# Optimization experiments

Hardware: AMD Instinct MI355X
Metric: run time of the kernel (lower is better)

## Reference

```python
import jax, jax.numpy as jnp
import numpy as np

EPS = 1e-5
HEADS = 16
DIM_HEAD = 64
ROPE_THETA = 10000.0


def layer_norm(x, g, b):
    mu = x.mean(-1, keepdims=True)
    var = x.var(-1, keepdims=True)
    return (x - mu) / jnp.sqrt(var + EPS) * g + b


def apply_rope(t):
    # t: [b, h, n, d]; interleaved-pair RoPE (rotary-embedding-torch default)
    n, d = t.shape[-2], t.shape[-1]
    inv_freq = 1.0 / (ROPE_THETA ** (jnp.arange(0, d, 2, dtype=jnp.float32) / d))  # [d/2]
    freqs = jnp.arange(n, dtype=jnp.float32)[:, None] * inv_freq[None, :]          # [n, d/2]
    freqs = jnp.repeat(freqs, 2, axis=-1)                                          # [n, d]
    cos, sin = jnp.cos(freqs).astype(t.dtype), jnp.sin(freqs).astype(t.dtype)
    t2 = t.reshape(*t.shape[:-1], d // 2, 2)
    t_rot = jnp.stack((-t2[..., 1], t2[..., 0]), axis=-1).reshape(t.shape)
    return t * cos + t_rot * sin


def setup_inputs() -> dict:
    key = jax.random.key(0)
    k0, k1, k2 = jax.random.split(key, 3)
    B, N, D = 1, 4096, 1024
    inner = HEADS * DIM_HEAD
    x = jax.random.normal(k0, (B, N, D), jnp.float32)
    w_qkv = jax.random.normal(k1, (D, inner * 3), jnp.float32) * (D ** -0.5)
    w_out = jax.random.normal(k2, (inner, D), jnp.float32) * (inner ** -0.5)
    ln_g = jnp.ones((D,), jnp.float32)
    ln_b = jnp.zeros((D,), jnp.float32)
    return {"x": x, "w_qkv": w_qkv, "w_out": w_out, "ln_g": ln_g, "ln_b": ln_b}


def reference(x, w_qkv, w_out, ln_g, ln_b):
    B, N, D = x.shape
    H, DH = HEADS, DIM_HEAD
    scale = DH ** -0.5

    h = layer_norm(x, ln_g, ln_b)
    qkv = h @ w_qkv                                    # [b, n, 3*inner]
    q, k, v = jnp.split(qkv, 3, axis=-1)
    to_heads = lambda t: t.reshape(B, N, H, DH).transpose(0, 2, 1, 3)  # [b,h,n,d]
    q, k, v = to_heads(q), to_heads(k), to_heads(v)

    new_k, new_v = k, v  # cache holds pre-RoPE k, v (as in original)

    q = apply_rope(q)
    k = apply_rope(k)

    dots = jnp.einsum('bhid,bhjd->bhij', q, k) * scale  # [b,h,n,n]
    causal_mask = jnp.triu(jnp.ones((N, N), dtype=bool), 1)
    dots = jnp.where(causal_mask, -jnp.inf, dots)
    attn = jax.nn.softmax(dots, axis=-1)
    out = jnp.einsum('bhij,bhjd->bhid', attn, v)        # [b,h,n,d]
    out = out.transpose(0, 2, 1, 3).reshape(B, N, H * DH)
    return out @ w_out, new_k, new_v
```

## Files before the change

### kernel.cpp

```cpp
#include <hip/hip_runtime.h>
#include <math.h>

#define D_MODEL 1024
#define N_SEQ   4096
#define N_HEADS 16
#define DHEAD   64
#define QKV_COLS 3072

typedef short bf16x8 __attribute__((ext_vector_type(8)));
typedef short bf16x4 __attribute__((ext_vector_type(4)));
typedef float f32x4  __attribute__((ext_vector_type(4)));

#define MFMA32(a, b, c) __builtin_amdgcn_mfma_f32_16x16x32_bf16(a, b, c, 0, 0, 0)
#define MFMA16(a, b, c) __builtin_amdgcn_mfma_f32_16x16x16bf16_1k(a, b, c, 0, 0, 0)

static __device__ __forceinline__ unsigned short f2bf(float f) {
    union { float f; unsigned u; } v; v.f = f;
    unsigned r = (v.u + 0x7fffu + ((v.u >> 16) & 1u)) >> 16;
    return (unsigned short)r;
}

static __device__ __forceinline__ bf16x4 pack_bf16x4(float a, float b, float c, float d) {
    union { float f; unsigned u; } x0, x1, x2, x3;
    x0.f = a; x1.f = b; x2.f = c; x3.f = d;
    union { unsigned u[2]; bf16x4 v; } r;
    r.u[0] = __builtin_amdgcn_perm(x1.u, x0.u, 0x07060302u);
    r.u[1] = __builtin_amdgcn_perm(x3.u, x2.u, 0x07060302u);
    return r.v;
}

typedef __attribute__((address_space(1))) const void* gas_t;
typedef __attribute__((address_space(3))) void* las_t;
static __device__ __forceinline__ void load_lds16(const unsigned short* g, unsigned short* l) {
    __builtin_amdgcn_global_load_lds((gas_t)g, (las_t)l, 16, 0, 0);
}

static __device__ __forceinline__ void fast_sincos(float theta, float* s, float* c) {
    float rev = theta * 0.15915494309189535f;
    rev = rev - floorf(rev);
    float a = rev * 6.283185307179586f;
    *s = __sinf(a);
    *c = __cosf(a);
}

__constant__ unsigned char U_TAB[80] = {
    71,65,59,54,49,45,40,36,31,27,23,19,15,11,7,3,
    69,63,57,52,48,43,39,34,30,26,22,18,14,10,6,2,
    67,61,55,51,46,42,37,33,29,25,21,17,13,9,5,1,
    70,68,66,64,53,50,47,44,28,24,20,16,79,78,77,76,
    56,58,60,62,32,35,38,41,0,4,8,12,72,73,74,75
};

__global__ __launch_bounds__(256) void ln_kernel(const float* __restrict__ x,
                                                 const float* __restrict__ g,
                                                 const float* __restrict__ b,
                                                 unsigned short* __restrict__ h) {
    int row = blockIdx.x;
    int t = threadIdx.x;
    float4 v = ((const float4*)(x + (size_t)row * D_MODEL))[t];
    float s  = v.x + v.y + v.z + v.w;
    float ss = v.x*v.x + v.y*v.y + v.z*v.z + v.w*v.w;
    for (int off = 32; off; off >>= 1) {
        s  += __shfl_down(s, off);
        ss += __shfl_down(ss, off);
    }
    __shared__ float sm[4], ssm[4];
    __shared__ float mu_s, rs_s;
    int wave = t >> 6, lane = t & 63;
    if (lane == 0) { sm[wave] = s; ssm[wave] = ss; }
    __syncthreads();
    if (t == 0) {
        float S = 0.f, SS = 0.f;
        for (int w = 0; w < 4; w++) { S += sm[w]; SS += ssm[w]; }
        float mu = S / D_MODEL;
        float var = SS / D_MODEL - mu * mu;
        mu_s = mu;
        rs_s = rsqrtf(var + 1e-5f);
    }
    __syncthreads();
    float mu = mu_s, rs = rs_s;
    float4 gv = ((const float4*)g)[t];
    float4 bv = ((const float4*)b)[t];
    ushort4 o;
    o.x = f2bf((v.x - mu) * rs * gv.x + bv.x);
    o.y = f2bf((v.y - mu) * rs * gv.y + bv.y);
    o.z = f2bf((v.z - mu) * rs * gv.z + bv.z);
    o.w = f2bf((v.w - mu) * rs * gv.w + bv.w);
    *(ushort4*)(h + (size_t)row * D_MODEL + t * 4) = o;
}

__global__ __launch_bounds__(256) void transpose_cvt2(const float* __restrict__ Wa,
                                                      unsigned short* __restrict__ Ta,
                                                      const float* __restrict__ Wb,
                                                      unsigned short* __restrict__ Tb) {
    __shared__ float tile[64][65];
    int by = blockIdx.y;
    const float* W; unsigned short* Wt; int N, n0;
    if (by < 48) { W = Wa; Wt = Ta; N = QKV_COLS; n0 = by * 64; }
    else         { W = Wb; Wt = Tb; N = D_MODEL;  n0 = (by - 48) * 64; }
    const int K = D_MODEL;
    int k0 = blockIdx.x * 64;
    int t = threadIdx.x;
#pragma unroll
    for (int p = 0; p < 16; p++) {
        int idx = p * 256 + t;
        int r = idx >> 6, c = idx & 63;
        tile[r][c] = W[(size_t)(k0 + r) * N + n0 + c];
    }
    __syncthreads();
#pragma unroll
    for (int p = 0; p < 16; p++) {
        int idx = p * 256 + t;
        int r2 = idx >> 6, c2 = idx & 63;
        Wt[(size_t)(n0 + r2) * K + k0 + c2] = f2bf(tile[c2][r2]);
    }
}

__global__ __launch_bounds__(256) void gemm_bt128(const unsigned short* __restrict__ A,
                                                  const unsigned short* __restrict__ Bt,
                                                  float* __restrict__ C,
                                                  int M, int N, int K) {
    __shared__ unsigned short As[128 * 32];
    __shared__ unsigned short Bs[128 * 32];
    int t = threadIdx.x;
    int w = t >> 6, lane = t & 63;
    int l16 = lane & 15, quad = lane >> 4;
    int wr = w >> 1, wc = w & 1;
    int m0 = blockIdx.x * 128, n0 = blockIdx.y * 128;
    int srow = lane >> 2, scol = (lane & 3) * 8;
    int c0 = w * 2, c1 = c0 + 1;

    f32x4 acc[4][4] = {};

    for (int k0 = 0; k0 < K; k0 += 32) {
        __syncthreads();
        load_lds16(A  + (size_t)(m0 + c0 * 16 + srow) * K + k0 + scol, &As[c0 * 512 + lane * 8]);
        load_lds16(A  + (size_t)(m0 + c1 * 16 + srow) * K + k0 + scol, &As[c1 * 512 + lane * 8]);
        load_lds16(Bt + (size_t)(n0 + c0 * 16 + srow) * K + k0 + scol, &Bs[c0 * 512 + lane * 8]);
        load_lds16(Bt + (size_t)(n0 + c1 * 16 + srow) * K + k0 + scol, &Bs[c1 * 512 + lane * 8]);
        __syncthreads();
        bf16x8 a[4], b[4];
#pragma unroll
        for (int mt = 0; mt < 4; mt++)
            a[mt] = *(const bf16x8*)&As[(wr * 64 + mt * 16 + l16) * 32 + quad * 8];
#pragma unroll
        for (int nt = 0; nt < 4; nt++)
            b[nt] = *(const bf16x8*)&Bs[(wc * 64 + nt * 16 + l16) * 32 + quad * 8];
#pragma unroll
        for (int mt = 0; mt < 4; mt++)
#pragma unroll
            for (int nt = 0; nt < 4; nt++)
                acc[mt][nt] = MFMA32(a[mt], b[nt], acc[mt][nt]);
    }
#pragma unroll
    for (int mt = 0; mt < 4; mt++)
#pragma unroll
        for (int nt = 0; nt < 4; nt++)
#pragma unroll
            for (int r = 0; r < 4; r++)
                C[(size_t)(m0 + wr * 64 + mt * 16 + quad * 4 + r) * N + n0 + wc * 64 + nt * 16 + l16] =
                    acc[mt][nt][r];
}

__global__ __launch_bounds__(256) void gemm_bt64(const unsigned short* __restrict__ A,
                                                 const unsigned short* __restrict__ Bt,
                                                 float* __restrict__ C,
                                                 int M, int N, int K) {
    __shared__ unsigned short As[64 * 32];
    __shared__ unsigned short Bs[128 * 32];
    int t = threadIdx.x;
    int w = t >> 6, lane = t & 63;
    int l16 = lane & 15, quad = lane >> 4;
    int wr = w >> 1, wc = w & 1;
    int m0 = blockIdx.x * 64, n0 = blockIdx.y * 128;
    int srow = lane >> 2, scol = (lane & 3) * 8;
    int c0 = w * 2, c1 = c0 + 1;
    int srow2 = t >> 2, scol2 = (t & 3) * 8;

    f32x4 acc[2][4] = {};

    for (int k0 = 0; k0 < K; k0 += 32) {
        __syncthreads();
        load_lds16(A  + (size_t)(m0 + srow2) * K + k0 + scol2, &As[t * 8]);
        load_lds16(Bt + (size_t)(n0 + c0 * 16 + srow) * K + k0 + scol, &Bs[c0 * 512 + lane * 8]);
        load_lds16(Bt + (size_t)(n0 + c1 * 16 + srow) * K + k0 + scol, &Bs[c1 * 512 + lane * 8]);
        __syncthreads();
        bf16x8 a[2], b[4];
#pragma unroll
        for (int mt = 0; mt < 2; mt++)
            a[mt] = *(const bf16x8*)&As[(wr * 32 + mt * 16 + l16) * 32 + quad * 8];
#pragma unroll
        for (int nt = 0; nt < 4; nt++)
            b[nt] = *(const bf16x8*)&Bs[(wc * 64 + nt * 16 + l16) * 32 + quad * 8];
#pragma unroll
        for (int mt = 0; mt < 2; mt++)
#pragma unroll
            for (int nt = 0; nt < 4; nt++)
                acc[mt][nt] = MFMA32(a[mt], b[nt], acc[mt][nt]);
    }
#pragma unroll
    for (int mt = 0; mt < 2; mt++)
#pragma unroll
        for (int nt = 0; nt < 4; nt++)
#pragma unroll
            for (int r = 0; r < 4; r++)
                C[(size_t)(m0 + wr * 32 + mt * 16 + quad * 4 + r) * N + n0 + wc * 64 + nt * 16 + l16] =
                    acc[mt][nt][r];
}

__global__ __launch_bounds__(256) void rope_cache_kernel(const float* __restrict__ qkv,
                                                         float* __restrict__ out_k,
                                                         float* __restrict__ out_v,
                                                         unsigned short* __restrict__ q_bf,
                                                         unsigned short* __restrict__ k_bf,
                                                         unsigned short* __restrict__ vt_bf) {
    __shared__ unsigned short Vt[64 * 72];
    int nt = blockIdx.x, h = blockIdx.y;
    int n0 = nt * 64;
    int t = threadIdx.x;
    int row = t >> 2;
    int n = n0 + row;
    const float* src = qkv + (size_t)n * QKV_COLS + h * 64;
    size_t nd_base = ((size_t)h * N_SEQ + n) * 64;
    const float QSCALE = 0.18033688011112042f;
    const float NL2_32 = -0.41524101186092029f;
#pragma unroll
    for (int j = 0; j < 4; j++) {
        int c = (t & 3) * 4 + j * 16;
        float4 q4 = *(const float4*)(src + c);
        float4 k4 = *(const float4*)(src + 1024 + c);
        float4 v4 = *(const float4*)(src + 2048 + c);
        *(float4*)(out_k + nd_base + c) = k4;
        *(float4*)(out_v + nd_base + c) = v4;
        float i0 = (float)(c >> 1), i1 = i0 + 1.f;
        float if0 = exp2f(i0 * NL2_32);
        float if1 = exp2f(i1 * NL2_32);
        float s0, c0s, s1, c1s;
        fast_sincos((float)n * if0, &s0, &c0s);
        fast_sincos((float)n * if1, &s1, &c1s);
        ushort4 qo, ko;
        qo.x = f2bf((q4.x * c0s - q4.y * s0) * QSCALE);
        qo.y = f2bf((q4.y * c0s + q4.x * s0) * QSCALE);
        qo.z = f2bf((q4.z * c1s - q4.w * s1) * QSCALE);
        qo.w = f2bf((q4.w * c1s + q4.z * s1) * QSCALE);
        ko.x = f2bf(k4.x * c0s - k4.y * s0); ko.y = f2bf(k4.y * c0s + k4.x * s0);
        ko.z = f2bf(k4.z * c1s - k4.w * s1); ko.w = f2bf(k4.w * c1s + k4.z * s1);
        *(ushort4*)(q_bf + nd_base + c) = qo;
        *(ushort4*)(k_bf + nd_base + c) = ko;
        ushort4 vo;
        vo.x = f2bf(v4.x); vo.y = f2bf(v4.y); vo.z = f2bf(v4.z); vo.w = f2bf(v4.w);
        *(ushort4*)&Vt[row * 72 + c] = vo;
    }
    __syncthreads();
    int d = t >> 2;
    int nb = (t & 3) * 16;
    unsigned short tmp[16];
#pragma unroll
    for (int i = 0; i < 16; i++) tmp[i] = Vt[(nb + i) * 72 + d];
    unsigned short* dst = vt_bf + ((size_t)h * DHEAD + d) * N_SEQ + n0 + nb;
#pragma unroll
    for (int i = 0; i < 16; i++) dst[i] = tmp[i];
}

__global__ __launch_bounds__(256, 3) void flash_mfma(const unsigned short* __restrict__ q_bf,
                                                     const unsigned short* __restrict__ k_bf,
                                                     const unsigned short* __restrict__ vt_bf,
                                                     unsigned short* __restrict__ attn_bf,
                                                     float* __restrict__ part_O,
                                                     float* __restrict__ part_l) {
    int idx = blockIdx.x;
    int h = idx & 15;
    int u = U_TAB[idx >> 4];
    int Qt, cc;
    bool partial = (u < 72);
    if (partial) {
        int r = 71 - u;
        if (r < 16)      { Qt = 8 + (r >> 1); cc = r & 1; }
        else if (r < 40) { int q3 = r - 16; int d3 = q3 / 3; Qt = 16 + d3; cc = q3 - 3 * d3; }
        else             { int q4 = r - 40; Qt = 24 + (q4 >> 2); cc = q4 & 3; }
    } else { Qt = 79 - u; cc = 0; }
    int kt0 = cc * 16;
    int kt_end = min(kt0 + 15, 2 * Qt + 1);

    int t = threadIdx.x;
    int w = t >> 6, lane = t & 63;
    int l16 = lane & 15, quad = lane >> 4;
    int sw = l16 & 7;

    __shared__ unsigned short Ks[2][4096];
    __shared__ unsigned short Vs[2][4096];

    int qr0 = Qt * 128 + w * 32;
    const unsigned short* Kg = k_bf + (size_t)h * N_SEQ * DHEAD;
    const unsigned short* Vg = vt_bf + (size_t)h * DHEAD * N_SEQ;

    bf16x8 bq[2][2];
#pragma unroll
    for (int qg = 0; qg < 2; qg++) {
        const unsigned short* qp = q_bf + ((size_t)h * N_SEQ + qr0 + qg * 16 + l16) * 64 + quad * 8;
        bq[qg][0] = *(const bf16x8*)(qp);
        bq[qg][1] = *(const bf16x8*)(qp + 32);
    }
    f32x4 O[2][4] = {};
    f32x4 Ol[2] = {};
    int my_kmax = (qr0 + 31) >> 6;

    int srow = t >> 3;
    int scol = ((t & 7) ^ (srow & 7)) * 8;

    int koffA[4], koffB[4];
#pragma unroll
    for (int tt = 0; tt < 4; tt++) {
        int krow = tt * 16 + l16;
        koffA[tt] = krow * 64 + ((quad ^ sw) * 8);
        koffB[tt] = krow * 64 + (((quad + 4) ^ sw) * 8);
    }
    int voff[4][4];
#pragma unroll
    for (int tt = 0; tt < 4; tt++)
#pragma unroll
        for (int dt = 0; dt < 4; dt++)
            voff[tt][dt] = (dt * 16 + l16) * 64 +
                           (((2 * tt + (quad >> 1)) ^ sw) * 8) + (quad & 1) * 4;

    const unsigned short* kg0 = Kg + (size_t)(kt0 * 64 + srow) * 64 + scol;
    const unsigned short* kg1 = kg0 + 2048;
    const unsigned short* vg0 = Vg + (size_t)srow * N_SEQ + kt0 * 64 + scol;
    const unsigned short* vg1 = vg0 + (size_t)32 * N_SEQ;

    const bf16x4 ones4 = {(short)0x3F80, (short)0x3F80, (short)0x3F80, (short)0x3F80};

    load_lds16(kg0, &Ks[0][t * 8]);
    load_lds16(kg1, &Ks[0][t * 8 + 2048]);
    load_lds16(vg0, &Vs[0][t * 8]);
    load_lds16(vg1, &Vs[0][t * 8 + 2048]);
    kg0 += 4096; kg1 += 4096; vg0 += 64; vg1 += 64;

    auto step = [&](int kt, const unsigned short* KC, const unsigned short* VC,
                    unsigned short* KN, unsigned short* VN) {
        __syncthreads();
        if (kt < kt_end) {
            load_lds16(kg0, KN + t * 8);
            load_lds16(kg1, KN + t * 8 + 2048);
            load_lds16(vg0, VN + t * 8);
            load_lds16(vg1, VN + t * 8 + 2048);
            kg0 += 4096; kg1 += 4096; vg0 += 64; vg1 += 64;
        }
        if (kt > my_kmax) return;
        int k0 = kt << 6;

        bf16x4 pf[2][4];
#pragma unroll
        for (int tt = 0; tt < 4; tt++) {
            int kbase = k0 + tt * 16;
            bf16x4 pz = (bf16x4){0, 0, 0, 0};
            if (kbase >= qr0 + 32) { pf[0][tt] = pz; pf[1][tt] = pz; continue; }
            bf16x8 kf0 = *(const bf16x8*)&KC[koffA[tt]];
            bf16x8 kf1 = *(const bf16x8*)&KC[koffB[tt]];
#pragma unroll
            for (int qg = 0; qg < 2; qg++) {
                int qb = qr0 + qg * 16;
                if (kbase > qb) { pf[qg][tt] = pz; continue; }
                f32x4 s = (f32x4){0.f, 0.f, 0.f, 0.f};
                s = MFMA32(kf0, bq[qg][0], s);
                s = MFMA32(kf1, bq[qg][1], s);
                float p0 = exp2f(s[0]);
                float p1 = exp2f(s[1]);
                float p2 = exp2f(s[2]);
                float p3 = exp2f(s[3]);
                if (kbase == qb) {
                    if (quad * 4 + 0 > l16) p0 = 0.f;
                    if (quad * 4 + 1 > l16) p1 = 0.f;
                    if (quad * 4 + 2 > l16) p2 = 0.f;
                    if (quad * 4 + 3 > l16) p3 = 0.f;
                }
                pf[qg][tt] = pack_bf16x4(p0, p1, p2, p3);
                Ol[qg] = MFMA16(ones4, pf[qg][tt], Ol[qg]);
            }
        }
        __builtin_amdgcn_s_setprio(1);
#pragma unroll
        for (int tt = 0; tt < 4; tt++) {
            if (k0 + tt * 16 < qr0 + 32) {
#pragma unroll
                for (int dt = 0; dt < 4; dt++) {
                    bf16x4 va = *(const bf16x4*)&VC[voff[tt][dt]];
                    O[0][dt] = MFMA16(va, pf[0][tt], O[0][dt]);
                    O[1][dt] = MFMA16(va, pf[1][tt], O[1][dt]);
                }
            }
        }
        __builtin_amdgcn_s_setprio(0);
    };

    for (int kt = kt0; kt <= kt_end; ) {
        step(kt, Ks[0], Vs[0], Ks[1], Vs[1]); kt++;
        if (kt > kt_end) break;
        step(kt, Ks[1], Vs[1], Ks[0], Vs[0]); kt++;
    }

#pragma unroll
    for (int qg = 0; qg < 2; qg++) {
        float l = Ol[qg][0];
        if (!partial) {
            float inv = 1.0f / l;
#pragma unroll
            for (int dt = 0; dt < 4; dt++) {
                ushort4 o;
                o.x = f2bf(O[qg][dt][0] * inv);
                o.y = f2bf(O[qg][dt][1] * inv);
                o.z = f2bf(O[qg][dt][2] * inv);
                o.w = f2bf(O[qg][dt][3] * inv);
                *(ushort4*)(attn_bf + (size_t)(qr0 + qg * 16 + l16) * D_MODEL + h * 64 + dt * 16 + quad * 4) = o;
            }
        } else {
            int uid = h * 72 + u;
            size_t ob = (size_t)uid * 8192;
            int qcol = w * 32 + qg * 16 + l16;
#pragma unroll
            for (int dt = 0; dt < 4; dt++)
#pragma unroll
                for (int r = 0; r < 4; r++)
                    part_O[ob + (size_t)(dt * 16 + quad * 4 + r) * 128 + qcol] = O[qg][dt][r];
            if (quad == 0) part_l[uid * 128 + qcol] = l;
        }
    }
}

__global__ __launch_bounds__(256) void combine_kernel(const float* __restrict__ part_O,
                                                      const float* __restrict__ part_l,
                                                      unsigned short* __restrict__ attn_bf) {
    int Qt = 8 + blockIdx.x;
    int h  = blockIdx.y;
    int nc = (Qt + 8) >> 3;
    int t = threadIdx.x;
    int q = t & 127;
    int dh = blockIdx.z * 32 + (t >> 7) * 16;
    float l = 0.f;
    float acc[16];
#pragma unroll
    for (int d = 0; d < 16; d++) acc[d] = 0.f;
    for (int c = 0; c < nc; c++) {
        int r;
        if (Qt < 16)      r = 2 * (Qt - 8) + c;
        else if (Qt < 24) r = 16 + 3 * (Qt - 16) + c;
        else              r = 40 + 4 * (Qt - 24) + c;
        int uid = h * 72 + (71 - r);
        l += part_l[uid * 128 + q];
        const float* po = part_O + (size_t)uid * 8192 + (size_t)dh * 128 + q;
#pragma unroll
        for (int d = 0; d < 16; d++) acc[d] += po[d * 128];
    }
    float inv = 1.0f / l;
    unsigned short* op = attn_bf + (size_t)(Qt * 128 + q) * D_MODEL + h * 64 + dh;
#pragma unroll
    for (int d = 0; d < 16; d++) op[d] = f2bf(acc[d] * inv);
}

extern "C" void kernel_launch(void* const* d_in, const int* in_sizes, int n_in,
                              void* d_out, int out_size, void* d_ws, size_t ws_size,
                              hipStream_t stream) {
    const float* x     = (const float*)d_in[0];
    const float* w_qkv = (const float*)d_in[1];
    const float* w_out = (const float*)d_in[2];
    const float* ln_g  = (const float*)d_in[3];
    const float* ln_b  = (const float*)d_in[4];

    float* out   = (float*)d_out;
    float* out_k = (float*)d_out + 4194304;
    float* out_v = (float*)d_out + 8388608;

    char* ws = (char*)d_ws;
    const size_t MiB = 1048576;
    float*          qkv_f   = (float*)(ws);
    unsigned short* h_bf    = (unsigned short*)(ws + 48*MiB);
    unsigned short* wqkvT   = (unsigned short*)(ws + 56*MiB);
    unsigned short* q_bf    = (unsigned short*)(ws + 48*MiB);
    unsigned short* k_bf    = (unsigned short*)(ws + 56*MiB);
    unsigned short* vt_bf   = (unsigned short*)(ws + 64*MiB);
    unsigned short* attn_bf = (unsigned short*)(ws);
    float*          part_l  = (float*)(ws + 8*MiB);
    float*          part_O  = (float*)(ws + 9*MiB);
    unsigned short* woutT   = (unsigned short*)(ws + 72*MiB);

    transpose_cvt2<<<dim3(16, 64), 256, 0, stream>>>(w_qkv, wqkvT, w_out, woutT);
    ln_kernel<<<N_SEQ, 256, 0, stream>>>(x, ln_g, ln_b, h_bf);
    gemm_bt128<<<dim3(32, 24), 256, 0, stream>>>(h_bf, wqkvT, qkv_f, N_SEQ, QKV_COLS, D_MODEL);
    rope_cache_kernel<<<dim3(64, 16), 256, 0, stream>>>(qkv_f, out_k, out_v, q_bf, k_bf, vt_bf);
    flash_mfma<<<1280, 256, 0, stream>>>(q_bf, k_bf, vt_bf, attn_bf, part_O, part_l);
    combine_kernel<<<dim3(24, 16, 2), 256, 0, stream>>>(part_O, part_l, attn_bf);
    gemm_bt64<<<dim3(64, 8), 256, 0, stream>>>(attn_bf, woutT, out, N_SEQ, D_MODEL, D_MODEL);
}
```

Baseline: 255.5 us.

## Read K/V fragments directly from global in flash kernel; merge LN and weight-transpose launches

```diff
diff --git a/kernel.cpp b/kernel.cpp
--- a/kernel.cpp
+++ b/kernel.cpp
@@ -51,68 +51,71 @@
     56,58,60,62,32,35,38,41,0,4,8,12,72,73,74,75
 };
 
-__global__ __launch_bounds__(256) void ln_kernel(const float* __restrict__ x,
-                                                 const float* __restrict__ g,
-                                                 const float* __restrict__ b,
-                                                 unsigned short* __restrict__ h) {
-    int row = blockIdx.x;
-    int t = threadIdx.x;
-    float4 v = ((const float4*)(x + (size_t)row * D_MODEL))[t];
-    float s  = v.x + v.y + v.z + v.w;
-    float ss = v.x*v.x + v.y*v.y + v.z*v.z + v.w*v.w;
-    for (int off = 32; off; off >>= 1) {
-        s  += __shfl_down(s, off);
-        ss += __shfl_down(ss, off);
-    }
-    __shared__ float sm[4], ssm[4];
-    __shared__ float mu_s, rs_s;
-    int wave = t >> 6, lane = t & 63;
-    if (lane == 0) { sm[wave] = s; ssm[wave] = ss; }
-    __syncthreads();
-    if (t == 0) {
-        float S = 0.f, SS = 0.f;
-        for (int w = 0; w < 4; w++) { S += sm[w]; SS += ssm[w]; }
-        float mu = S / D_MODEL;
-        float var = SS / D_MODEL - mu * mu;
-        mu_s = mu;
-        rs_s = rsqrtf(var + 1e-5f);
-    }
-    __syncthreads();
-    float mu = mu_s, rs = rs_s;
-    float4 gv = ((const float4*)g)[t];
-    float4 bv = ((const float4*)b)[t];
-    ushort4 o;
-    o.x = f2bf((v.x - mu) * rs * gv.x + bv.x);
-    o.y = f2bf((v.y - mu) * rs * gv.y + bv.y);
-    o.z = f2bf((v.z - mu) * rs * gv.z + bv.z);
-    o.w = f2bf((v.w - mu) * rs * gv.w + bv.w);
-    *(ushort4*)(h + (size_t)row * D_MODEL + t * 4) = o;
-}
-
-__global__ __launch_bounds__(256) void transpose_cvt2(const float* __restrict__ Wa,
-                                                      unsigned short* __restrict__ Ta,
-                                                      const float* __restrict__ Wb,
-                                                      unsigned short* __restrict__ Tb) {
+__global__ __launch_bounds__(256) void prep_kernel(const float* __restrict__ x,
+                                                   const float* __restrict__ g,
+                                                   const float* __restrict__ b,
+                                                   unsigned short* __restrict__ hb,
+                                                   const float* __restrict__ Wa,
+                                                   unsigned short* __restrict__ Ta,
+                                                   const float* __restrict__ Wb,
+                                                   unsigned short* __restrict__ Tb) {
     __shared__ float tile[64][65];
-    int by = blockIdx.y;
-    const float* W; unsigned short* Wt; int N, n0;
-    if (by < 48) { W = Wa; Wt = Ta; N = QKV_COLS; n0 = by * 64; }
-    else         { W = Wb; Wt = Tb; N = D_MODEL;  n0 = (by - 48) * 64; }
-    const int K = D_MODEL;
-    int k0 = blockIdx.x * 64;
-    int t = threadIdx.x;
-#pragma unroll
-    for (int p = 0; p < 16; p++) {
-        int idx = p * 256 + t;
-        int r = idx >> 6, c = idx & 63;
-        tile[r][c] = W[(size_t)(k0 + r) * N + n0 + c];
-    }
-    __syncthreads();
-#pragma unroll
-    for (int p = 0; p < 16; p++) {
-        int idx = p * 256 + t;
-        int r2 = idx >> 6, c2 = idx & 63;
-        Wt[(size_t)(n0 + r2) * K + k0 + c2] = f2bf(tile[c2][r2]);
+    int bid = blockIdx.x;
+    int t = threadIdx.x;
+    if (bid < 4096) {
+        int row = bid;
+        float4 v = ((const float4*)(x + (size_t)row * D_MODEL))[t];
+        float s  = v.x + v.y + v.z + v.w;
+        float ss = v.x*v.x + v.y*v.y + v.z*v.z + v.w*v.w;
+        for (int off = 32; off; off >>= 1) {
+            s  += __shfl_down(s, off);
+            ss += __shfl_down(ss, off);
+        }
+        float* sm  = &tile[0][0];
+        float* ssm = &tile[0][8];
+        float* mu_rs = &tile[0][16];
+        int wave = t >> 6, lane = t & 63;
+        if (lane == 0) { sm[wave] = s; ssm[wave] = ss; }
+        __syncthreads();
+        if (t == 0) {
+            float S = 0.f, SS = 0.f;
+            for (int w2 = 0; w2 < 4; w2++) { S += sm[w2]; SS += ssm[w2]; }
+            float mu = S / D_MODEL;
+            float var = SS / D_MODEL - mu * mu;
+            mu_rs[0] = mu;
+            mu_rs[1] = rsqrtf(var + 1e-5f);
+        }
+        __syncthreads();
+        float mu = mu_rs[0], rs = mu_rs[1];
+        float4 gv = ((const float4*)g)[t];
+        float4 bv = ((const float4*)b)[t];
+        ushort4 o;
+        o.x = f2bf((v.x - mu) * rs * gv.x + bv.x);
+        o.y = f2bf((v.y - mu) * rs * gv.y + bv.y);
+        o.z = f2bf((v.z - mu) * rs * gv.z + bv.z);
+        o.w = f2bf((v.w - mu) * rs * gv.w + bv.w);
+        *(ushort4*)(hb + (size_t)row * D_MODEL + t * 4) = o;
+    } else {
+        int r = bid - 4096;
+        int by = r >> 4, bx = r & 15;
+        const float* W; unsigned short* Wt; int N, n0;
+        if (by < 48) { W = Wa; Wt = Ta; N = QKV_COLS; n0 = by * 64; }
+        else         { W = Wb; Wt = Tb; N = D_MODEL;  n0 = (by - 48) * 64; }
+        const int K = D_MODEL;
+        int k0 = bx * 64;
+#pragma unroll
+        for (int p = 0; p < 16; p++) {
+            int idx = p * 256 + t;
+            int rr = idx >> 6, c = idx & 63;
+            tile[rr][c] = W[(size_t)(k0 + rr) * N + n0 + c];
+        }
+        __syncthreads();
+#pragma unroll
+        for (int p = 0; p < 16; p++) {
+            int idx = p * 256 + t;
+            int r2 = idx >> 6, c2 = idx & 63;
+            Wt[(size_t)(n0 + r2) * K + k0 + c2] = f2bf(tile[c2][r2]);
+        }
     }
 }
 
@@ -262,7 +265,7 @@
     for (int i = 0; i < 16; i++) dst[i] = tmp[i];
 }
 
-__global__ __launch_bounds__(256, 3) void flash_mfma(const unsigned short* __restrict__ q_bf,
+__global__ __launch_bounds__(256, 4) void flash_mfma(const unsigned short* __restrict__ q_bf,
                                                      const unsigned short* __restrict__ k_bf,
                                                      const unsigned short* __restrict__ vt_bf,
                                                      unsigned short* __restrict__ attn_bf,
@@ -285,10 +288,6 @@
     int t = threadIdx.x;
     int w = t >> 6, lane = t & 63;
     int l16 = lane & 15, quad = lane >> 4;
-    int sw = l16 & 7;
-
-    __shared__ unsigned short Ks[2][4096];
-    __shared__ unsigned short Vs[2][4096];
 
     int qr0 = Qt * 128 + w * 32;
     const unsigned short* Kg = k_bf + (size_t)h * N_SEQ * DHEAD;
@@ -304,63 +303,27 @@
     f32x4 O[2][4] = {};
     f32x4 Ol[2] = {};
     int my_kmax = (qr0 + 31) >> 6;
-
-    int srow = t >> 3;
-    int scol = ((t & 7) ^ (srow & 7)) * 8;
-
-    int koffA[4], koffB[4];
-#pragma unroll
-    for (int tt = 0; tt < 4; tt++) {
-        int krow = tt * 16 + l16;
-        koffA[tt] = krow * 64 + ((quad ^ sw) * 8);
-        koffB[tt] = krow * 64 + (((quad + 4) ^ sw) * 8);
-    }
-    int voff[4][4];
-#pragma unroll
-    for (int tt = 0; tt < 4; tt++)
-#pragma unroll
-        for (int dt = 0; dt < 4; dt++)
-            voff[tt][dt] = (dt * 16 + l16) * 64 +
-                           (((2 * tt + (quad >> 1)) ^ sw) * 8) + (quad & 1) * 4;
-
-    const unsigned short* kg0 = Kg + (size_t)(kt0 * 64 + srow) * 64 + scol;
-    const unsigned short* kg1 = kg0 + 2048;
-    const unsigned short* vg0 = Vg + (size_t)srow * N_SEQ + kt0 * 64 + scol;
-    const unsigned short* vg1 = vg0 + (size_t)32 * N_SEQ;
+    int kt_hi = min(kt_end, my_kmax);
+
+    const unsigned short* kbase = Kg + (size_t)(kt0 * 64 + l16) * 64 + quad * 8;
+    const unsigned short* vbase = Vg + (size_t)l16 * N_SEQ + kt0 * 64 + quad * 4;
 
     const bf16x4 ones4 = {(short)0x3F80, (short)0x3F80, (short)0x3F80, (short)0x3F80};
 
-    load_lds16(kg0, &Ks[0][t * 8]);
-    load_lds16(kg1, &Ks[0][t * 8 + 2048]);
-    load_lds16(vg0, &Vs[0][t * 8]);
-    load_lds16(vg1, &Vs[0][t * 8 + 2048]);
-    kg0 += 4096; kg1 += 4096; vg0 += 64; vg1 += 64;
-
-    auto step = [&](int kt, const unsigned short* KC, const unsigned short* VC,
-                    unsigned short* KN, unsigned short* VN) {
-        __syncthreads();
-        if (kt < kt_end) {
-            load_lds16(kg0, KN + t * 8);
-            load_lds16(kg1, KN + t * 8 + 2048);
-            load_lds16(vg0, VN + t * 8);
-            load_lds16(vg1, VN + t * 8 + 2048);
-            kg0 += 4096; kg1 += 4096; vg0 += 64; vg1 += 64;
-        }
-        if (kt > my_kmax) return;
+    for (int kt = kt0; kt <= kt_hi; kt++) {
         int k0 = kt << 6;
-
         bf16x4 pf[2][4];
 #pragma unroll
         for (int tt = 0; tt < 4; tt++) {
-            int kbase = k0 + tt * 16;
+            int kbase_k = k0 + tt * 16;
             bf16x4 pz = (bf16x4){0, 0, 0, 0};
-            if (kbase >= qr0 + 32) { pf[0][tt] = pz; pf[1][tt] = pz; continue; }
-            bf16x8 kf0 = *(const bf16x8*)&KC[koffA[tt]];
-            bf16x8 kf1 = *(const bf16x8*)&KC[koffB[tt]];
+            if (kbase_k >= qr0 + 32) { pf[0][tt] = pz; pf[1][tt] = pz; continue; }
+            bf16x8 kf0 = *(const bf16x8*)(kbase + tt * 1024);
+            bf16x8 kf1 = *(const bf16x8*)(kbase + tt * 1024 + 32);
 #pragma unroll
             for (int qg = 0; qg < 2; qg++) {
                 int qb = qr0 + qg * 16;
-                if (kbase > qb) { pf[qg][tt] = pz; continue; }
+                if (kbase_k > qb) { pf[qg][tt] = pz; continue; }
                 f32x4 s = (f32x4){0.f, 0.f, 0.f, 0.f};
                 s = MFMA32(kf0, bq[qg][0], s);
                 s = MFMA32(kf1, bq[qg][1], s);
@@ -368,7 +331,7 @@
                 float p1 = exp2f(s[1]);
                 float p2 = exp2f(s[2]);
                 float p3 = exp2f(s[3]);
-                if (kbase == qb) {
+                if (kbase_k == qb) {
                     if (quad * 4 + 0 > l16) p0 = 0.f;
                     if (quad * 4 + 1 > l16) p1 = 0.f;
                     if (quad * 4 + 2 > l16) p2 = 0.f;
@@ -384,19 +347,15 @@
             if (k0 + tt * 16 < qr0 + 32) {
 #pragma unroll
                 for (int dt = 0; dt < 4; dt++) {
-                    bf16x4 va = *(const bf16x4*)&VC[voff[tt][dt]];
+                    bf16x4 va = *(const bf16x4*)(vbase + (size_t)dt * 16 * N_SEQ + tt * 16);
                     O[0][dt] = MFMA16(va, pf[0][tt], O[0][dt]);
                     O[1][dt] = MFMA16(va, pf[1][tt], O[1][dt]);
                 }
             }
         }
         __builtin_amdgcn_s_setprio(0);
-    };
-
-    for (int kt = kt0; kt <= kt_end; ) {
-        step(kt, Ks[0], Vs[0], Ks[1], Vs[1]); kt++;
-        if (kt > kt_end) break;
-        step(kt, Ks[1], Vs[1], Ks[0], Vs[0]); kt++;
+        kbase += 4096;
+        vbase += 64;
     }
 
 #pragma unroll
@@ -483,8 +442,7 @@
     float*          part_O  = (float*)(ws + 9*MiB);
     unsigned short* woutT   = (unsigned short*)(ws + 72*MiB);
 
-    transpose_cvt2<<<dim3(16, 64), 256, 0, stream>>>(w_qkv, wqkvT, w_out, woutT);
-    ln_kernel<<<N_SEQ, 256, 0, stream>>>(x, ln_g, ln_b, h_bf);
+    prep_kernel<<<5120, 256, 0, stream>>>(x, ln_g, ln_b, h_bf, w_qkv, wqkvT, w_out, woutT);
     gemm_bt128<<<dim3(32, 24), 256, 0, stream>>>(h_bf, wqkvT, qkv_f, N_SEQ, QKV_COLS, D_MODEL);
     rope_cache_kernel<<<dim3(64, 16), 256, 0, stream>>>(qkv_f, out_k, out_v, q_bf, k_bf, vt_bf);
     flash_mfma<<<1280, 256, 0, stream>>>(q_bf, k_bf, vt_bf, attn_bf, part_O, part_l);
```

Measured after the change: 376.0 us. +47.2%, slower.
